# Kernel tuning notes

Hardware: AMD Instinct MI355X
Metric: run time of the kernel (lower is better)

## Reference

```python
import jax, jax.numpy as jnp
import numpy as np

EPS = 1e-8  # undefined global EPS in source; standard small epsilon


def setup_inputs() -> dict:
    key = jax.random.key(0)
    k1, k2 = jax.random.split(key)
    B, C = 262144, 128
    inp = jax.random.uniform(k1, (B, C), dtype=jnp.float32)
    tgt = jax.random.uniform(k2, (B, C), dtype=jnp.float32)
    return {"input": inp, "target": tgt}


def reference(input, target):
    # res = -sum_{i,x} input[i,x] * log(target[i,x] + eps); return [res / B]
    B = input.shape[0]
    res = -jnp.sum(input * jnp.log(target + EPS))
    return jnp.stack([res / B])
```

## Files before the change

kernel.cpp:

```cpp
#include <hip/hip_runtime.h>


constexpr int BLOCK = 256;
constexpr int GRID  = 2048;

__global__ __launch_bounds__(BLOCK) void cce_reduce_kernel(
    const float* __restrict__ inp, const float* __restrict__ tgt,
    float* __restrict__ out, int n4, float neg_inv_b) {
  const float4* __restrict__ in4 = reinterpret_cast<const float4*>(inp);
  const float4* __restrict__ tg4 = reinterpret_cast<const float4*>(tgt);

  const int idx    = blockIdx.x * BLOCK + threadIdx.x;
  const int stride = GRID * BLOCK;

  float acc0 = 0.0f, acc1 = 0.0f;

  int i = idx;
  for (; i + 3 * stride < n4; i += 4 * stride) {
    float4 x0 = in4[i];
    float4 y0 = tg4[i];
    float4 x1 = in4[i + stride];
    float4 y1 = tg4[i + stride];
    float4 x2 = in4[i + 2 * stride];
    float4 y2 = tg4[i + 2 * stride];
    float4 x3 = in4[i + 3 * stride];
    float4 y3 = tg4[i + 3 * stride];

    acc0 += x0.x * __logf(y0.x + 1e-8f);
    acc1 += x0.y * __logf(y0.y + 1e-8f);
    acc0 += x0.z * __logf(y0.z + 1e-8f);
    acc1 += x0.w * __logf(y0.w + 1e-8f);
    acc0 += x1.x * __logf(y1.x + 1e-8f);
    acc1 += x1.y * __logf(y1.y + 1e-8f);
    acc0 += x1.z * __logf(y1.z + 1e-8f);
    acc1 += x1.w * __logf(y1.w + 1e-8f);
    acc0 += x2.x * __logf(y2.x + 1e-8f);
    acc1 += x2.y * __logf(y2.y + 1e-8f);
    acc0 += x2.z * __logf(y2.z + 1e-8f);
    acc1 += x2.w * __logf(y2.w + 1e-8f);
    acc0 += x3.x * __logf(y3.x + 1e-8f);
    acc1 += x3.y * __logf(y3.y + 1e-8f);
    acc0 += x3.z * __logf(y3.z + 1e-8f);
    acc1 += x3.w * __logf(y3.w + 1e-8f);
  }
  for (; i < n4; i += stride) {
    float4 x = in4[i];
    float4 y = tg4[i];
    acc0 += x.x * __logf(y.x + 1e-8f);
    acc1 += x.y * __logf(y.y + 1e-8f);
    acc0 += x.z * __logf(y.z + 1e-8f);
    acc1 += x.w * __logf(y.w + 1e-8f);
  }

  float acc = acc0 + acc1;

  #pragma unroll
  for (int off = 32; off > 0; off >>= 1)
    acc += __shfl_down(acc, off, 64);

  __shared__ float s[BLOCK / 64];
  const int lane = threadIdx.x & 63;
  const int wave = threadIdx.x >> 6;
  if (lane == 0) s[wave] = acc;
  __syncthreads();

  if (threadIdx.x == 0) {
    float t = 0.0f;
    #pragma unroll
    for (int w = 0; w < BLOCK / 64; ++w) t += s[w];
    atomicAdd(out, t * neg_inv_b);
  }
}

extern "C" void kernel_launch(void* const* d_in, const int* in_sizes, int n_in,
                              void* d_out, int out_size, void* d_ws, size_t ws_size,
                              hipStream_t stream) {
  const float* inp = reinterpret_cast<const float*>(d_in[0]);
  const float* tgt = reinterpret_cast<const float*>(d_in[1]);
  float* out = reinterpret_cast<float*>(d_out);

  const long long n = (long long)in_sizes[0];
  const int n4 = (int)(n / 4);
  const long long B = 262144;
  const float neg_inv_b = -1.0f / (float)B;

  hipMemsetAsync(d_out, 0, out_size * sizeof(float), stream);

  cce_reduce_kernel<<<GRID, BLOCK, 0, stream>>>(inp, tgt, out, n4, neg_inv_b);
}
```

Before: 274.8 us.

## Software-pipeline loads with register double-buffering and halve grid size

```diff
diff --git a/kernel.cpp b/kernel.cpp
--- a/kernel.cpp
+++ b/kernel.cpp
@@ -2,9 +2,9 @@
 
 
 constexpr int BLOCK = 256;
-constexpr int GRID  = 2048;
+constexpr int GRID  = 1024;
 
-__global__ __launch_bounds__(BLOCK) void cce_reduce_kernel(
+__global__ __launch_bounds__(BLOCK, 4) void cce_reduce_kernel(
     const float* __restrict__ inp, const float* __restrict__ tgt,
     float* __restrict__ out, int n4, float neg_inv_b) {
   const float4* __restrict__ in4 = reinterpret_cast<const float4*>(inp);
@@ -12,47 +12,45 @@
 
   const int idx    = blockIdx.x * BLOCK + threadIdx.x;
   const int stride = GRID * BLOCK;
+  const int step   = 4 * stride;
 
-  float acc0 = 0.0f, acc1 = 0.0f;
+  float acc0 = 0.f, acc1 = 0.f, acc2 = 0.f, acc3 = 0.f;
+
+#define TERM4(X, Y)                        \
+  acc0 += (X).x * __logf((Y).x + 1e-8f);   \
+  acc1 += (X).y * __logf((Y).y + 1e-8f);   \
+  acc2 += (X).z * __logf((Y).z + 1e-8f);   \
+  acc3 += (X).w * __logf((Y).w + 1e-8f);
 
   int i = idx;
-  for (; i + 3 * stride < n4; i += 4 * stride) {
-    float4 x0 = in4[i];
-    float4 y0 = tg4[i];
-    float4 x1 = in4[i + stride];
-    float4 y1 = tg4[i + stride];
-    float4 x2 = in4[i + 2 * stride];
-    float4 y2 = tg4[i + 2 * stride];
-    float4 x3 = in4[i + 3 * stride];
-    float4 y3 = tg4[i + 3 * stride];
+  if (i + 7 * stride < n4) {
+    float4 ax0 = in4[i],              ay0 = tg4[i];
+    float4 ax1 = in4[i + stride],     ay1 = tg4[i + stride];
+    float4 ax2 = in4[i + 2 * stride], ay2 = tg4[i + 2 * stride];
+    float4 ax3 = in4[i + 3 * stride], ay3 = tg4[i + 3 * stride];
+    i += step;
 
-    acc0 += x0.x * __logf(y0.x + 1e-8f);
-    acc1 += x0.y * __logf(y0.y + 1e-8f);
-    acc0 += x0.z * __logf(y0.z + 1e-8f);
-    acc1 += x0.w * __logf(y0.w + 1e-8f);
-    acc0 += x1.x * __logf(y1.x + 1e-8f);
-    acc1 += x1.y * __logf(y1.y + 1e-8f);
-    acc0 += x1.z * __logf(y1.z + 1e-8f);
-    acc1 += x1.w * __logf(y1.w + 1e-8f);
-    acc0 += x2.x * __logf(y2.x + 1e-8f);
-    acc1 += x2.y * __logf(y2.y + 1e-8f);
-    acc0 += x2.z * __logf(y2.z + 1e-8f);
-    acc1 += x2.w * __logf(y2.w + 1e-8f);
-    acc0 += x3.x * __logf(y3.x + 1e-8f);
-    acc1 += x3.y * __logf(y3.y + 1e-8f);
-    acc0 += x3.z * __logf(y3.z + 1e-8f);
-    acc1 += x3.w * __logf(y3.w + 1e-8f);
+    for (; i + 3 * stride < n4; i += step) {
+      float4 bx0 = in4[i],              by0 = tg4[i];
+      float4 bx1 = in4[i + stride],     by1 = tg4[i + stride];
+      float4 bx2 = in4[i + 2 * stride], by2 = tg4[i + 2 * stride];
+      float4 bx3 = in4[i + 3 * stride], by3 = tg4[i + 3 * stride];
+      __builtin_amdgcn_sched_barrier(0);
+
+      TERM4(ax0, ay0) TERM4(ax1, ay1) TERM4(ax2, ay2) TERM4(ax3, ay3)
+
+      ax0 = bx0; ay0 = by0; ax1 = bx1; ay1 = by1;
+      ax2 = bx2; ay2 = by2; ax3 = bx3; ay3 = by3;
+    }
+    TERM4(ax0, ay0) TERM4(ax1, ay1) TERM4(ax2, ay2) TERM4(ax3, ay3)
   }
   for (; i < n4; i += stride) {
-    float4 x = in4[i];
-    float4 y = tg4[i];
-    acc0 += x.x * __logf(y.x + 1e-8f);
-    acc1 += x.y * __logf(y.y + 1e-8f);
-    acc0 += x.z * __logf(y.z + 1e-8f);
-    acc1 += x.w * __logf(y.w + 1e-8f);
+    float4 x = in4[i], y = tg4[i];
+    TERM4(x, y)
   }
+#undef TERM4
 
-  float acc = acc0 + acc1;
+  float acc = (acc0 + acc1) + (acc2 + acc3);
 
   #pragma unroll
   for (int off = 32; off > 0; off >>= 1)
```

Result: no change. 275.3 us (+0.2%).
